# Kernel optimization log

Hardware: AMD Instinct MI355X
Metric: run time of the kernel (lower is better)

Reference implementation:

```python
import jax, jax.numpy as jnp
import numpy as np

IN_MODES = (4, 4, 8, 8, 4)
OUT_MODES = (4, 4, 8, 8, 4)
RANKS = (1, 8, 8, 8, 8, 1)
N_TOKENS = 8192


def setup_inputs() -> dict:
    key = jax.random.key(0)
    ks = jax.random.split(key, 7)
    inp = jax.random.normal(ks[0], (N_TOKENS, int(np.prod(IN_MODES))), dtype=jnp.float32)
    cores = []
    for i in range(5):
        shape = (IN_MODES[i], RANKS[i], RANKS[i + 1], OUT_MODES[i])
        # kaiming-uniform-like small init to keep the 5-core chain numerically tame
        fan_in = shape[0] * shape[1] * shape[2]
        bound = float(np.sqrt(3.0 / fan_in))
        cores.append(jax.random.uniform(ks[i + 1], shape, minval=-bound, maxval=bound, dtype=jnp.float32))
    biases = jax.random.uniform(ks[6], (int(np.prod(OUT_MODES)),), minval=-0.05, maxval=0.05, dtype=jnp.float32)
    return {
        "input": inp,
        "core0": cores[0], "core1": cores[1], "core2": cores[2],
        "core3": cores[3], "core4": cores[4],
        "biases": biases,
    }


def reference(input, core0, core1, core2, core3, core4, biases):
    # reshape tokens into the 5 input modes: [N, a, b, c, d, e]
    x = input.reshape((-1,) + IN_MODES)
    # TT contraction. Original einsum has no '->'; free indices h (ranks[0]=1)
    # and m (ranks[5]=1) are size-1 boundary ranks, so summing them out here is
    # equivalent to the original reshape-squeeze.
    out = jnp.einsum(
        'nabcde,ahiv,bijw,cjkx,dkly,elmz->nvwxyz',
        x, core0, core1, core2, core3, core4,
        optimize='optimal',
    )
    out = out.reshape(-1, int(np.prod(OUT_MODES)))
    return out + biases
```

## Files before the change

### kernel.cpp

```cpp
#include <hip/hip_runtime.h>

#define DIM 4096

typedef __bf16 bf16x8 __attribute__((ext_vector_type(8)));
typedef float floatx4 __attribute__((ext_vector_type(4)));

__device__ __forceinline__ void async_ld16(void* lds, const void* g) {
  __builtin_amdgcn_global_load_lds(
      (const __attribute__((address_space(1))) unsigned int*)g,
      (__attribute__((address_space(3))) unsigned int*)lds, 16, 0, 0);
}

__global__ void build_k(const float* __restrict__ c0, const float* __restrict__ c1,
                        const float* __restrict__ c2, const float* __restrict__ c3,
                        const float* __restrict__ c4,
                        float* __restrict__ K012, float* __restrict__ K34T) {
  const int bid = blockIdx.x, tid = threadIdx.x;
  if (bid < 512) {
    __shared__ float K01s[128];
    const int abc = bid >> 2;
    const int ab = abc >> 3, c = abc & 7;
    if (tid < 128) {
      const int a = ab >> 2, b = ab & 3;
      const int j = tid >> 4, vw = tid & 15, v = vw >> 2, w = vw & 3;
      float s = 0.f;
#pragma unroll
      for (int i = 0; i < 8; ++i)
        s += c0[a * 32 + i * 4 + v] * c1[b * 256 + i * 32 + j * 4 + w];
      K01s[tid] = s;
    }
    __syncthreads();
    const int t = bid * 256 + tid;
    const int vwx = t & 127, k = (t >> 7) & 7;
    const int vw = vwx >> 3, xx = vwx & 7;
    float s = 0.f;
#pragma unroll
    for (int j = 0; j < 8; ++j)
      s += K01s[j * 16 + vw] * c2[c * 512 + j * 64 + k * 8 + xx];
    K012[t] = s;
  } else {
    const int u = (bid - 512) * 256 + tid;
    const int yz = u & 31, kk = (u >> 5) & 7, de = u >> 8;
    const int d = de >> 2, e = de & 3, y = yz >> 2, z = yz & 3;
    float s = 0.f;
#pragma unroll
    for (int l = 0; l < 8; ++l)
      s += c3[d * 512 + kk * 64 + l * 8 + y] * c4[e * 32 + l * 4 + z];
    K34T[kk * 1024 + yz * 32 + de] = s;
  }
}

__global__ void build_wt_conv(const float* __restrict__ K012, const float* __restrict__ K34T,
                              __bf16* __restrict__ WT,
                              const float* __restrict__ X, __bf16* __restrict__ Xb) {
  const int bid = blockIdx.x, tid = threadIdx.x;
  if (bid < 8192) {
    const long t = (long)bid * 256 + tid;
    const long e8 = t * 8;
    const int in = (int)(e8 & 4095), o = (int)(e8 >> 12);
    const int de0 = in & 31, abc = in >> 5;
    const int yz = o & 31, vwx = o >> 5;
    const float* kp = K012 + abc * 1024 + vwx;
    const float* vp = K34T + yz * 32 + de0;
    float s[8] = {};
#pragma unroll
    for (int k = 0; k < 8; ++k) {
      const float a = kp[k * 128];
      const float4 v0 = *(const float4*)(vp + k * 1024);
      const float4 v1 = *(const float4*)(vp + k * 1024 + 4);
      s[0] += a * v0.x; s[1] += a * v0.y; s[2] += a * v0.z; s[3] += a * v0.w;
      s[4] += a * v1.x; s[5] += a * v1.y; s[6] += a * v1.z; s[7] += a * v1.w;
    }
    bf16x8 w;
#pragma unroll
    for (int d = 0; d < 8; ++d) w[d] = (__bf16)s[d];
    ((bf16x8*)WT)[t] = w;
  } else {
    const long t = (long)(bid - 8192) * 256 + tid;
    const float4 a = ((const float4*)X)[t * 2];
    const float4 b = ((const float4*)X)[t * 2 + 1];
    bf16x8 w;
    w[0] = (__bf16)a.x; w[1] = (__bf16)a.y; w[2] = (__bf16)a.z; w[3] = (__bf16)a.w;
    w[4] = (__bf16)b.x; w[5] = (__bf16)b.y; w[6] = (__bf16)b.z; w[7] = (__bf16)b.w;
    ((bf16x8*)Xb)[t] = w;
  }
}


#define SB0()  __builtin_amdgcn_sched_barrier(0)
#define BARO() do { __builtin_amdgcn_s_barrier(); SB0(); } while (0)
#define ENDPH() do { asm volatile("s_waitcnt vmcnt(6)" ::: "memory"); \
                     __builtin_amdgcn_s_barrier(); SB0(); } while (0)
#define P1() __builtin_amdgcn_s_setprio(1)
#define P0() __builtin_amdgcn_s_setprio(0)

#define STA(p, h, koff) do { \
  async_ld16(&As[p][(h) * 128][0] + ldsq[0], agp[0] + (h) * 524288 + (koff)); \
  async_ld16(&As[p][(h) * 128][0] + ldsq[1], agp[1] + (h) * 524288 + (koff)); } while (0)
#define STB(p, h, koff) do { \
  async_ld16(&Bs[p][(h) * 128][0] + ldsq[0], bgp[0] + (h) * 524288 + (koff)); \
  async_ld16(&Bs[p][(h) * 128][0] + ldsq[1], bgp[1] + (h) * 524288 + (koff)); } while (0)

#define RDA2(p, mh, f0) do { \
  _Pragma("unroll") for (int fi = (f0); fi < (f0) + 2; ++fi) { \
    const int row = ((mh) * 8 + 2 * fi + wm) * 16 + lm; \
    _Pragma("unroll") for (int kh = 0; kh < 2; ++kh) \
      af[fi][kh] = *(const bf16x8*)&As[p][row][((kh * 4 + kq) ^ (row & 7)) * 8]; \
  } } while (0)
#define RDB1(p, nh, sl, gi) do { \
  const int row = (4 * ((nh) * 2 + (gi)) + wn) * 16 + lm; \
  _Pragma("unroll") for (int kh = 0; kh < 2; ++kh) \
    bs[sl][gi][kh] = *(const bf16x8*)&Bs[p][row][((kh * 4 + kq) ^ (row & 7)) * 8]; \
  } while (0)

#define MMA8F(sl, mh, nh, f0) do { \
  _Pragma("unroll") for (int fi = (f0); fi < (f0) + 2; ++fi) \
  _Pragma("unroll") for (int gi = 0; gi < 2; ++gi) \
  _Pragma("unroll") for (int kh = 0; kh < 2; ++kh) \
    acc[(mh) * 4 + fi][(nh) * 2 + gi] = __builtin_amdgcn_mfma_f32_16x16x32_bf16( \
        af[fi][kh], bs[sl][gi][kh], acc[(mh) * 4 + fi][(nh) * 2 + gi], 0, 0, 0); } while (0)
#define MMA8G(sl, mh, nh, gi) do { \
  _Pragma("unroll") for (int fi = 0; fi < 4; ++fi) \
  _Pragma("unroll") for (int kh = 0; kh < 2; ++kh) \
    acc[(mh) * 4 + fi][(nh) * 2 + (gi)] = __builtin_amdgcn_mfma_f32_16x16x32_bf16( \
        af[fi][kh], bs[sl][gi][kh], acc[(mh) * 4 + fi][(nh) * 2 + (gi)], 0, 0, 0); } while (0)
#define MMA16(sl, mh, nh) do { \
  _Pragma("unroll") for (int fi = 0; fi < 4; ++fi) \
  _Pragma("unroll") for (int gi = 0; gi < 2; ++gi) \
  _Pragma("unroll") for (int kh = 0; kh < 2; ++kh) \
    acc[(mh) * 4 + fi][(nh) * 2 + gi] = __builtin_amdgcn_mfma_f32_16x16x32_bf16( \
        af[fi][kh], bs[sl][gi][kh], acc[(mh) * 4 + fi][(nh) * 2 + gi], 0, 0, 0); } while (0)

__global__ __launch_bounds__(512, 2) void gemm_8ph(const __bf16* __restrict__ A,
                                                   const __bf16* __restrict__ WT,
                                                   const float* __restrict__ bias,
                                                   float* __restrict__ C) {
  __shared__ __bf16 As[2][256][64];
  __shared__ __bf16 Bs[2][256][64];

  const int tid = threadIdx.x;
  const int gb = (blockIdx.x & 7) * 64 + (blockIdx.x >> 3);
  const int m0 = (gb >> 4) * 256;
  const int n0 = (gb & 15) * 256;

  const int wave = tid >> 6, lane = tid & 63;
  const int wm = wave & 1, wn = wave >> 1;
  const int lm = lane & 15, kq = lane >> 4;

  floatx4 acc[8][4] = {};
  bf16x8 af[4][2], bs[2][2][2];

  const __bf16* agp[2];
  const __bf16* bgp[2];
  int ldsq[2];
#pragma unroll
  for (int j = 0; j < 2; ++j) {
    const int q = tid + j * 512;
    const int r = q >> 3, pc = q & 7;
    const int c = pc ^ (r & 7);
    ldsq[j] = q * 8;
    agp[j] = A + (long)(m0 + r) * DIM + c * 8;
    bgp[j] = WT + (long)(n0 + r) * DIM + c * 8;
  }

  STB(0, 0, 0); STA(0, 0, 0); STB(0, 1, 0); STA(0, 1, 0); STB(1, 0, 64);
  asm volatile("s_waitcnt vmcnt(6)" ::: "memory");
  __builtin_amdgcn_s_barrier();
  SB0();
  RDB1(0, 0, 1, 0); RDB1(0, 0, 1, 1);

#pragma unroll 1
  for (int it = 0; it < 32; ++it) {
    const int kE1 = (2 * it + 1) * 64;
    int t2 = 2 * it + 2; if (t2 > 63) t2 = 63;
    int t3 = 2 * it + 3; if (t3 > 63) t3 = 63;
    const int k2 = t2 * 64, k3 = t3 * 64;

    RDA2(0, 0, 0); SB0(); RDA2(0, 0, 2); STA(1, 0, kE1);
    BARO(); P1(); MMA8F(1, 0, 0, 0); SB0(); MMA8F(1, 0, 0, 2); P0();
    ENDPH();

    RDB1(0, 1, 0, 0); SB0(); RDB1(0, 1, 0, 1); STB(1, 1, kE1);
    BARO(); P1(); MMA8G(0, 0, 1, 0); SB0(); MMA8G(0, 0, 1, 1); P0();
    ENDPH();

    RDA2(0, 1, 0); SB0(); RDA2(0, 1, 2); STA(1, 1, kE1);
    BARO(); P1(); MMA8F(0, 1, 1, 0); SB0(); MMA8F(0, 1, 1, 2); P0();
    ENDPH();

    RDB1(1, 0, 0, 0); SB0(); RDB1(1, 0, 0, 1); STB(0, 0, k2);
    BARO(); P1(); MMA16(1, 1, 0); P0();
    ENDPH();

    RDA2(1, 0, 0); SB0(); RDA2(1, 0, 2); STA(0, 0, k2);
    BARO(); P1(); MMA8F(0, 0, 0, 0); SB0(); MMA8F(0, 0, 0, 2); P0();
    ENDPH();

    RDB1(1, 1, 1, 0); SB0(); RDB1(1, 1, 1, 1); STB(0, 1, k2);
    BARO(); P1(); MMA8G(1, 0, 1, 0); SB0(); MMA8G(1, 0, 1, 1); P0();
    ENDPH();

    RDA2(1, 1, 0); SB0(); RDA2(1, 1, 2); STA(0, 1, k2);
    BARO(); P1(); MMA8F(1, 1, 1, 0); SB0(); MMA8F(1, 1, 1, 2); P0();
    ENDPH();

    RDB1(0, 0, 1, 0); SB0(); RDB1(0, 0, 1, 1); STB(1, 0, k3);
    BARO(); P1(); MMA16(0, 1, 0); P0();
    ENDPH();
  }

  float bv[4];
#pragma unroll
  for (int g = 0; g < 4; ++g) bv[g] = bias[n0 + (4 * g + wn) * 16 + lm];
#pragma unroll
  for (int f = 0; f < 8; ++f) {
    const long mr = m0 + (2 * f + wm) * 16 + kq * 4;
#pragma unroll
    for (int g = 0; g < 4; ++g) {
      float* cp = C + mr * DIM + n0 + (4 * g + wn) * 16 + lm;
      cp[0]       = acc[f][g][0] + bv[g];
      cp[DIM]     = acc[f][g][1] + bv[g];
      cp[2 * DIM] = acc[f][g][2] + bv[g];
      cp[3 * DIM] = acc[f][g][3] + bv[g];
    }
  }
}

__global__ __launch_bounds__(256) void gemm_xw(const float* __restrict__ X,
                                               const __bf16* __restrict__ WT,
                                               const float* __restrict__ bias,
                                               float* __restrict__ C) {
  __shared__ __bf16 Asf[128 * 40];
  __shared__ __bf16 Bsf[128 * 32];

  const int tid = threadIdx.x;
  const int n0 = (blockIdx.x & 31) * 128;
  const int m0 = (blockIdx.x >> 5) * 128;

  const int wave = tid >> 6, lane = tid & 63;
  const int wm = (wave >> 1) * 64, wn = (wave & 1) * 64;
  const int lm = lane & 15, kq = lane >> 4;

  floatx4 acc[4][4] = {};

  const int ar = tid >> 1;
  const int ac = (tid & 1) * 16;
  const float* xp = X + (long)(m0 + ar) * DIM + ac;
  __bf16* as_dst = &Asf[ar * 40 + ac];

  const int u0 = tid, u1 = 256 + tid;
  const int r0 = u0 >> 2, r1 = u1 >> 2;
  const int ch0 = (u0 & 3) ^ (r0 & 3), ch1 = (u1 & 3) ^ (r1 & 3);
  const __bf16* wp0 = WT + (long)(n0 + r0) * DIM + ch0 * 8;
  const __bf16* wp1 = WT + (long)(n0 + r1) * DIM + ch1 * 8;

  float4 a0 = *(const float4*)(xp);
  float4 a1 = *(const float4*)(xp + 4);
  float4 a2 = *(const float4*)(xp + 8);
  float4 a3 = *(const float4*)(xp + 12);

#pragma unroll 1
  for (int k0 = 0; k0 < DIM; k0 += 32) {
    async_ld16(&Bsf[u0 * 8], wp0 + k0);
    async_ld16(&Bsf[u1 * 8], wp1 + k0);

    bf16x8 w0, w1;
    w0[0] = (__bf16)a0.x; w0[1] = (__bf16)a0.y; w0[2] = (__bf16)a0.z; w0[3] = (__bf16)a0.w;
    w0[4] = (__bf16)a1.x; w0[5] = (__bf16)a1.y; w0[6] = (__bf16)a1.z; w0[7] = (__bf16)a1.w;
    w1[0] = (__bf16)a2.x; w1[1] = (__bf16)a2.y; w1[2] = (__bf16)a2.z; w1[3] = (__bf16)a2.w;
    w1[4] = (__bf16)a3.x; w1[5] = (__bf16)a3.y; w1[6] = (__bf16)a3.z; w1[7] = (__bf16)a3.w;
    *(bf16x8*)(as_dst) = w0;
    *(bf16x8*)(as_dst + 8) = w1;

    if (k0 + 32 < DIM) {
      a0 = *(const float4*)(xp + k0 + 32);
      a1 = *(const float4*)(xp + k0 + 36);
      a2 = *(const float4*)(xp + k0 + 40);
      a3 = *(const float4*)(xp + k0 + 44);
    }
    __syncthreads();

    bf16x8 afv[4], bfr[4];
#pragma unroll
    for (int mi = 0; mi < 4; ++mi)
      afv[mi] = *(const bf16x8*)&Asf[(wm + mi * 16 + lm) * 40 + kq * 8];
#pragma unroll
    for (int ni = 0; ni < 4; ++ni) {
      int rr = wn + ni * 16 + lm;
      bfr[ni] = *(const bf16x8*)&Bsf[rr * 32 + ((kq ^ (rr & 3)) * 8)];
    }
#pragma unroll
    for (int mi = 0; mi < 4; ++mi)
#pragma unroll
      for (int ni = 0; ni < 4; ++ni)
        acc[mi][ni] = __builtin_amdgcn_mfma_f32_16x16x32_bf16(afv[mi], bfr[ni], acc[mi][ni], 0, 0, 0);
    __syncthreads();
  }

  float bv[4];
#pragma unroll
  for (int ni = 0; ni < 4; ++ni) bv[ni] = bias[n0 + wn + ni * 16 + lm];
#pragma unroll
  for (int mi = 0; mi < 4; ++mi) {
    long mr = m0 + wm + mi * 16 + kq * 4;
#pragma unroll
    for (int ni = 0; ni < 4; ++ni) {
      float* cp = C + mr * DIM + (n0 + wn + ni * 16 + lm);
      cp[0]       = acc[mi][ni][0] + bv[ni];
      cp[DIM]     = acc[mi][ni][1] + bv[ni];
      cp[2 * DIM] = acc[mi][ni][2] + bv[ni];
      cp[3 * DIM] = acc[mi][ni][3] + bv[ni];
    }
  }
}

extern "C" void kernel_launch(void* const* d_in, const int* in_sizes, int n_in,
                              void* d_out, int out_size, void* d_ws, size_t ws_size,
                              hipStream_t stream) {
  const float* x    = (const float*)d_in[0];
  const float* c0   = (const float*)d_in[1];
  const float* c1   = (const float*)d_in[2];
  const float* c2   = (const float*)d_in[3];
  const float* c3   = (const float*)d_in[4];
  const float* c4   = (const float*)d_in[5];
  const float* bias = (const float*)d_in[6];
  float* out = (float*)d_out;

  const size_t XB_SZ = 67108864;
  const size_t WT_SZ = 33554432;
  const size_t K012_SZ = 524288;
  const size_t K34_SZ = 32768;
  char* ws = (char*)d_ws;

  if (ws_size >= XB_SZ + WT_SZ + K012_SZ + K34_SZ) {
    __bf16* Xb  = (__bf16*)ws;
    __bf16* WT  = (__bf16*)(ws + XB_SZ);
    float* K012 = (float*)(ws + XB_SZ + WT_SZ);
    float* K34T = (float*)(ws + XB_SZ + WT_SZ + K012_SZ);

    build_k<<<544, 256, 0, stream>>>(c0, c1, c2, c3, c4, K012, K34T);
    build_wt_conv<<<24576, 256, 0, stream>>>(K012, K34T, WT, x, Xb);
    gemm_8ph<<<512, 512, 0, stream>>>(Xb, WT, bias, out);
  } else {
    __bf16* WT  = (__bf16*)ws;
    float* K012 = (float*)(ws + WT_SZ);
    float* K34T = (float*)(ws + WT_SZ + K012_SZ);

    build_k<<<544, 256, 0, stream>>>(c0, c1, c2, c3, c4, K012, K34T);
    build_wt_conv<<<8192, 256, 0, stream>>>(K012, K34T, WT, x, (__bf16*)nullptr);
    gemm_xw<<<2048, 256, 0, stream>>>(x, WT, bias, out);
  }
}
```

Baseline: 500.4 us.

## Restructure GEMM main loop to prefetch a full K-tile ahead with per-tile waits

Reworks the 8-phase bf16 MFMA main loop so that global-to-LDS async loads run a whole K-tile (two stages) ahead. The prologue now issues all loads for the first two tiles. The vmcnt wait moves from every phase to once per K-tile, and each phase waits explicitly on lgkmcnt(0) before its MFMAs. This is meant to cut the per-phase memory stalls and barrier overhead. It adds a second barrier in most phases, and ordering the writes into buffers that are still being read is delicate.

```diff
diff --git a/kernel.cpp b/kernel.cpp
--- a/kernel.cpp
+++ b/kernel.cpp
@@ -88,9 +88,9 @@
 
 
 #define SB0()  __builtin_amdgcn_sched_barrier(0)
-#define BARO() do { __builtin_amdgcn_s_barrier(); SB0(); } while (0)
-#define ENDPH() do { asm volatile("s_waitcnt vmcnt(6)" ::: "memory"); \
-                     __builtin_amdgcn_s_barrier(); SB0(); } while (0)
+#define LGKM0() asm volatile("s_waitcnt lgkmcnt(0)" ::: "memory")
+#define VM6()  asm volatile("s_waitcnt vmcnt(6)" ::: "memory")
+#define BAR()  __builtin_amdgcn_s_barrier()
 #define P1() __builtin_amdgcn_s_setprio(1)
 #define P0() __builtin_amdgcn_s_setprio(0)
 
@@ -101,30 +101,20 @@
   async_ld16(&Bs[p][(h) * 128][0] + ldsq[0], bgp[0] + (h) * 524288 + (koff)); \
   async_ld16(&Bs[p][(h) * 128][0] + ldsq[1], bgp[1] + (h) * 524288 + (koff)); } while (0)
 
-#define RDA2(p, mh, f0) do { \
-  _Pragma("unroll") for (int fi = (f0); fi < (f0) + 2; ++fi) { \
+#define RDA(p, mh) do { \
+  _Pragma("unroll") for (int fi = 0; fi < 4; ++fi) { \
     const int row = ((mh) * 8 + 2 * fi + wm) * 16 + lm; \
     _Pragma("unroll") for (int kh = 0; kh < 2; ++kh) \
       af[fi][kh] = *(const bf16x8*)&As[p][row][((kh * 4 + kq) ^ (row & 7)) * 8]; \
   } } while (0)
-#define RDB1(p, nh, sl, gi) do { \
-  const int row = (4 * ((nh) * 2 + (gi)) + wn) * 16 + lm; \
-  _Pragma("unroll") for (int kh = 0; kh < 2; ++kh) \
-    bs[sl][gi][kh] = *(const bf16x8*)&Bs[p][row][((kh * 4 + kq) ^ (row & 7)) * 8]; \
-  } while (0)
-
-#define MMA8F(sl, mh, nh, f0) do { \
-  _Pragma("unroll") for (int fi = (f0); fi < (f0) + 2; ++fi) \
-  _Pragma("unroll") for (int gi = 0; gi < 2; ++gi) \
-  _Pragma("unroll") for (int kh = 0; kh < 2; ++kh) \
-    acc[(mh) * 4 + fi][(nh) * 2 + gi] = __builtin_amdgcn_mfma_f32_16x16x32_bf16( \
-        af[fi][kh], bs[sl][gi][kh], acc[(mh) * 4 + fi][(nh) * 2 + gi], 0, 0, 0); } while (0)
-#define MMA8G(sl, mh, nh, gi) do { \
-  _Pragma("unroll") for (int fi = 0; fi < 4; ++fi) \
-  _Pragma("unroll") for (int kh = 0; kh < 2; ++kh) \
-    acc[(mh) * 4 + fi][(nh) * 2 + (gi)] = __builtin_amdgcn_mfma_f32_16x16x32_bf16( \
-        af[fi][kh], bs[sl][gi][kh], acc[(mh) * 4 + fi][(nh) * 2 + (gi)], 0, 0, 0); } while (0)
-#define MMA16(sl, mh, nh) do { \
+#define RDB(p, nh, sl) do { \
+  _Pragma("unroll") for (int gi = 0; gi < 2; ++gi) { \
+    const int row = (4 * ((nh) * 2 + gi) + wn) * 16 + lm; \
+    _Pragma("unroll") for (int kh = 0; kh < 2; ++kh) \
+      bs[sl][gi][kh] = *(const bf16x8*)&Bs[p][row][((kh * 4 + kq) ^ (row & 7)) * 8]; \
+  } } while (0)
+
+#define MMAQ(sl, mh, nh) do { \
   _Pragma("unroll") for (int fi = 0; fi < 4; ++fi) \
   _Pragma("unroll") for (int gi = 0; gi < 2; ++gi) \
   _Pragma("unroll") for (int kh = 0; kh < 2; ++kh) \
@@ -164,49 +154,46 @@
   }
 
   STB(0, 0, 0); STA(0, 0, 0); STB(0, 1, 0); STA(0, 1, 0); STB(1, 0, 64);
-  asm volatile("s_waitcnt vmcnt(6)" ::: "memory");
-  __builtin_amdgcn_s_barrier();
-  SB0();
-  RDB1(0, 0, 1, 0); RDB1(0, 0, 1, 1);
+  STA(1, 0, 64); STB(1, 1, 64); STA(1, 1, 64);
+  VM6();
+  BAR(); SB0();
+  RDB(0, 0, 0);
 
 #pragma unroll 1
   for (int it = 0; it < 32; ++it) {
-    const int kE1 = (2 * it + 1) * 64;
     int t2 = 2 * it + 2; if (t2 > 63) t2 = 63;
     int t3 = 2 * it + 3; if (t3 > 63) t3 = 63;
     const int k2 = t2 * 64, k3 = t3 * 64;
 
-    RDA2(0, 0, 0); SB0(); RDA2(0, 0, 2); STA(1, 0, kE1);
-    BARO(); P1(); MMA8F(1, 0, 0, 0); SB0(); MMA8F(1, 0, 0, 2); P0();
-    ENDPH();
-
-    RDB1(0, 1, 0, 0); SB0(); RDB1(0, 1, 0, 1); STB(1, 1, kE1);
-    BARO(); P1(); MMA8G(0, 0, 1, 0); SB0(); MMA8G(0, 0, 1, 1); P0();
-    ENDPH();
-
-    RDA2(0, 1, 0); SB0(); RDA2(0, 1, 2); STA(1, 1, kE1);
-    BARO(); P1(); MMA8F(0, 1, 1, 0); SB0(); MMA8F(0, 1, 1, 2); P0();
-    ENDPH();
-
-    RDB1(1, 0, 0, 0); SB0(); RDB1(1, 0, 0, 1); STB(0, 0, k2);
-    BARO(); P1(); MMA16(1, 1, 0); P0();
-    ENDPH();
-
-    RDA2(1, 0, 0); SB0(); RDA2(1, 0, 2); STA(0, 0, k2);
-    BARO(); P1(); MMA8F(0, 0, 0, 0); SB0(); MMA8F(0, 0, 0, 2); P0();
-    ENDPH();
-
-    RDB1(1, 1, 1, 0); SB0(); RDB1(1, 1, 1, 1); STB(0, 1, k2);
-    BARO(); P1(); MMA8G(1, 0, 1, 0); SB0(); MMA8G(1, 0, 1, 1); P0();
-    ENDPH();
-
-    RDA2(1, 1, 0); SB0(); RDA2(1, 1, 2); STA(0, 1, k2);
-    BARO(); P1(); MMA8F(1, 1, 1, 0); SB0(); MMA8F(1, 1, 1, 2); P0();
-    ENDPH();
-
-    RDB1(0, 0, 1, 0); SB0(); RDB1(0, 0, 1, 1); STB(1, 0, k3);
-    BARO(); P1(); MMA16(0, 1, 0); P0();
-    ENDPH();
+    RDA(0, 0); STB(0, 0, k2);
+    BAR(); LGKM0(); SB0(); P1(); MMAQ(0, 0, 0); P0(); BAR(); SB0();
+
+    RDB(0, 1, 1); STA(0, 0, k2);
+    BAR(); LGKM0(); SB0(); P1(); MMAQ(1, 0, 1); P0(); BAR(); SB0();
+
+    RDA(0, 1); STB(0, 1, k2);
+    BAR(); LGKM0(); SB0(); P1(); MMAQ(1, 1, 1); P0(); BAR(); SB0();
+
+    RDB(1, 0, 1); STA(0, 1, k2);
+    BAR(); SB0(); P1(); MMAQ(0, 1, 0); P0();
+    LGKM0();
+    VM6();
+    BAR(); SB0();
+
+    RDA(1, 0); STB(1, 0, k3);
+    BAR(); LGKM0(); SB0(); P1(); MMAQ(1, 0, 0); P0(); BAR(); SB0();
+
+    RDB(1, 1, 0); STA(1, 0, k3);
+    BAR(); LGKM0(); SB0(); P1(); MMAQ(0, 0, 1); P0(); BAR(); SB0();
+
+    RDA(1, 1); STB(1, 1, k3);
+    BAR(); LGKM0(); SB0(); P1(); MMAQ(0, 1, 1); P0(); BAR(); SB0();
+
+    RDB(0, 0, 0); STA(1, 1, k3);
+    BAR(); SB0(); P1(); MMAQ(1, 1, 0); P0();
+    LGKM0();
+    VM6();
+    BAR(); SB0();
   }
 
   float bv[4];
```

After: 491.7 us. About the same (-1.7%).
